# Kernel tuning notes

Hardware: AMD Instinct MI355X
Metric: run time of the kernel (lower is better)

The kernel has to match this reference:

```python
import jax, jax.numpy as jnp
import numpy as np

N, E, F, H1, H2 = 8192, 131072, 512, 32, 16
POS_WEIGHT = 10.0


def gcn_conv(x, W, src, dst, n):
    h = x @ W  # [n, out]
    deg = jax.ops.segment_sum(jnp.ones(dst.shape[0], x.dtype), dst, num_segments=n) + 1.0  # self-loop
    dinv = jnp.where(deg > 0, deg ** -0.5, 0.0)
    coef = dinv[src] * dinv[dst]  # [E]
    out = jax.ops.segment_sum(h[src] * coef[:, None], dst, num_segments=n)
    out = out + h * (dinv * dinv)[:, None]  # self-loop message
    return out


def setup_inputs() -> dict:
    key = jax.random.key(0)
    ks = jax.random.split(key, 8)
    x = jax.random.normal(ks[0], (N, F), dtype=jnp.float32)
    edge_index = jax.random.randint(ks[1], (2, E), 0, N, dtype=jnp.int32)
    adj_label = jax.random.randint(ks[2], (N, N), 0, 2, dtype=jnp.int32)
    eps = jax.random.normal(ks[3], (N, H2), dtype=jnp.float32)
    norm = jnp.ones((1,), dtype=jnp.float32)
    W1 = jax.random.normal(ks[4], (F, H1), dtype=jnp.float32) * 0.05
    W2 = jax.random.normal(ks[5], (H1, H2), dtype=jnp.float32) * 0.05
    W3 = jax.random.normal(ks[6], (H1, H2), dtype=jnp.float32) * 0.05
    return {"x": x, "edge_index": edge_index, "adj_label": adj_label,
            "eps": eps, "norm": norm, "W1": W1, "W2": W2, "W3": W3}


def reference(x, edge_index, adj_label, eps, norm, W1, W2, W3):
    n = x.shape[0]
    src, dst = edge_index[0], edge_index[1]
    h1 = jax.nn.relu(gcn_conv(x, W1, src, dst, n))
    mu = gcn_conv(h1, W2, src, dst, n)
    logvar = gcn_conv(h1, W3, src, dst, n)
    # reparameterize: std = exp(logvar) (as in source, not exp(0.5*logvar))
    z = eps * jnp.exp(logvar) + mu
    logits = z @ z.T  # [N, N] inner-product decode
    y = adj_label.astype(logits.dtype)
    # BCEWithLogitsLoss with pos_weight, numerically stable
    sp = jax.nn.softplus(-logits)
    bce = jnp.mean(POS_WEIGHT * y * sp + (1.0 - y) * (logits + sp))
    cost = norm[0] * bce
    kld = (-0.5 / n) * jnp.mean(jnp.sum(1.0 + 2.0 * logvar - mu ** 2 - jnp.exp(logvar) ** 2, axis=1))
    return cost + kld, mu
```

## Files before the change

### kernel.cpp

```cpp
#include <hip/hip_runtime.h>
#include <cstdint>
#include <cstddef>

#define N_NODES 8192
#define N_EDGES 131072
#define F_IN    512
#define H1C     32
#define H2C     16


__device__ __forceinline__ float block_reduce_sum(float v, int nthreads) {
    #pragma unroll
    for (int off = 32; off; off >>= 1) v += __shfl_down(v, off, 64);
    __shared__ float sred[16];
    int lane = threadIdx.x & 63, wid = threadIdx.x >> 6;
    if (lane == 0) sred[wid] = v;
    __syncthreads();
    float s = 0.0f;
    if (threadIdx.x == 0) {
        int nw = nthreads >> 6;
        for (int i = 0; i < nw; ++i) s += sred[i];
    }
    return s;
}

__device__ __forceinline__ float bce_elem(float l, int y) {
    float lse = __logf(1.0f + __expf(-fabsf(l)));
    float sp  = lse + fmaxf(l, 0.0f);
    float w   = (float)y;
    return fmaf(sp, fmaf(9.0f, w, 1.0f), -10.0f * w * l);
}


__global__ void k_init(float4* __restrict__ p) {
    int gid = blockIdx.x * 256 + threadIdx.x;
    float4 zz = {0.0f, 0.0f, 0.0f, 0.0f};
    p[gid] = zz;
}

__global__ void k_fill(const int* __restrict__ src, const int* __restrict__ dst,
                       int* __restrict__ cnt, int* __restrict__ csr_src) {
    int e = blockIdx.x * 256 + threadIdx.x;
    int d = dst[e], sv = src[e];
    int slot = atomicAdd(&cnt[d], 1);
    if (slot < 64) csr_src[(d << 6) + slot] = sv;
}

__global__ void __launch_bounds__(256)
k_gemm1(const float* __restrict__ x, const float* __restrict__ W1,
        float* __restrict__ h) {
    __shared__ float wsm[F_IN][H1C];
    int tid = threadIdx.x;
    {
        float4* wd = (float4*)wsm;
        const float4* wsrc = (const float4*)W1;
        #pragma unroll
        for (int i = 0; i < 16; ++i) wd[tid + i * 256] = wsrc[tid + i * 256];
    }
    __syncthreads();

    int row = (blockIdx.x << 5) + (tid >> 3);
    int c4 = (tid & 7) << 2;
    const float4* xp = (const float4*)&x[(size_t)row * F_IN];

    float ax = 0.f, ay = 0.f, az = 0.f, aw = 0.f;
    #pragma unroll 8
    for (int k4 = 0; k4 < F_IN / 4; ++k4) {
        float4 xv = xp[k4];
        float4 w0 = *(const float4*)&wsm[k4 * 4 + 0][c4];
        float4 w1 = *(const float4*)&wsm[k4 * 4 + 1][c4];
        float4 w2 = *(const float4*)&wsm[k4 * 4 + 2][c4];
        float4 w3 = *(const float4*)&wsm[k4 * 4 + 3][c4];
        ax = fmaf(xv.x, w0.x, ax); ay = fmaf(xv.x, w0.y, ay);
        az = fmaf(xv.x, w0.z, az); aw = fmaf(xv.x, w0.w, aw);
        ax = fmaf(xv.y, w1.x, ax); ay = fmaf(xv.y, w1.y, ay);
        az = fmaf(xv.y, w1.z, az); aw = fmaf(xv.y, w1.w, aw);
        ax = fmaf(xv.z, w2.x, ax); ay = fmaf(xv.z, w2.y, ay);
        az = fmaf(xv.z, w2.z, az); aw = fmaf(xv.z, w2.w, aw);
        ax = fmaf(xv.w, w3.x, ax); ay = fmaf(xv.w, w3.y, ay);
        az = fmaf(xv.w, w3.z, az); aw = fmaf(xv.w, w3.w, aw);
    }
    float4 v; v.x = ax; v.y = ay; v.z = az; v.w = aw;
    *(float4*)&h[(size_t)row * H1C + c4] = v;
}

__global__ void __launch_bounds__(256)
k_g1g2(const int* __restrict__ csr_src, const int* __restrict__ cnt,
       const float* __restrict__ h, const float* __restrict__ W2,
       const float* __restrict__ W3, float* __restrict__ h2mu,
       float* __restrict__ h2lv) {
    __shared__ float w2s[H1C * H2C], w3s[H1C * H2C];
    __shared__ float h1s[4][33];
    int tid = threadIdx.x;
    {
        w2s[tid] = W2[tid]; w2s[tid + 256] = W2[tid + 256];
        w3s[tid] = W3[tid]; w3s[tid + 256] = W3[tid + 256];
    }
    __syncthreads();

    int w = tid >> 6;
    int row = blockIdx.x * 4 + w;
    int lane = tid & 63;
    int f = lane & 31, half = lane >> 5;
    int n = min(cnt[row], 64);
    float acc = 0.0f;
    for (int sl = half; sl < n; sl += 2) {
        int s = csr_src[(row << 6) + sl];
        float c = rsqrtf((float)(cnt[s] + 1));
        acc = fmaf(h[(s << 5) + f], c, acc);
    }
    acc += __shfl_down(acc, 32, 64);
    if (half == 0) {
        float di = rsqrtf((float)(n + 1)), d2 = di * di;
        float a1 = acc * di;
        h1s[w][f] = fmaxf(fmaf(h[(row << 5) + f], d2, a1), 0.0f);
    }
    if (half == 0) {
        const float* wsrc = (f < 16) ? w2s : w3s;
        int col = f & 15;
        float o = 0.0f;
        #pragma unroll
        for (int k = 0; k < H1C; ++k) o = fmaf(h1s[w][k], wsrc[(k << 4) + col], o);
        if (f < 16) h2mu[(row << 4) + col] = o;
        else        h2lv[(row << 4) + col] = o;
    }
}

__global__ void __launch_bounds__(256)
k_g2z(const int* __restrict__ csr_src, const int* __restrict__ cnt,
      const float* __restrict__ h2mu, const float* __restrict__ h2lv,
      const float* __restrict__ eps, float* __restrict__ zbuf,
      float* __restrict__ out, float* __restrict__ kldp) {
    int tid = threadIdx.x;
    int row = blockIdx.x * 4 + (tid >> 6);
    int lane = tid & 63;
    int f = lane & 31, half = lane >> 5;
    int ff = f & 15;
    const float* hsrc = (f < 16) ? h2mu : h2lv;
    int n = min(cnt[row], 64);
    float acc = 0.0f;
    for (int sl = half; sl < n; sl += 2) {
        int s = csr_src[(row << 6) + sl];
        float c = rsqrtf((float)(cnt[s] + 1));
        acc = fmaf(hsrc[(s << 4) + ff], c, acc);
    }
    acc += __shfl_down(acc, 32, 64);
    float di = rsqrtf((float)(n + 1)), d2 = di * di;
    float val = fmaf(hsrc[(row << 4) + ff], d2, acc * di);
    float other = __shfl_xor(val, 16, 64);
    float kterm = 0.0f;
    if (half == 0 && f < 16) {
        float m = val, lv = other;
        float el = __expf(lv);
        float zv = fmaf(eps[(row << 4) + ff], el, m);
        zbuf[(row << 4) + ff] = zv;
        out[1 + (row << 4) + ff] = m;
        kterm = 1.0f + 2.0f * lv - m * m - el * el;
    }
    float bs = block_reduce_sum(kterm, 256);
    if (tid == 0) kldp[blockIdx.x] = bs;
}

__global__ void __launch_bounds__(256)
k_bce(const float* __restrict__ z, const int* __restrict__ adj,
      float* __restrict__ part) {
    __shared__ float zrT[16][32];
    int tid = threadIdx.x;
    int band = blockIdx.x & 15;
    int rblk = blockIdx.x >> 4;
    int col0 = (band << 9) + (tid << 1);
    int row0 = rblk << 5;

    if (tid < 128) {
        int r = tid >> 2, q = (tid & 3) << 2;
        float4 v = *(const float4*)&z[(size_t)(row0 + r) * H2C + q];
        zrT[q + 0][r] = v.x; zrT[q + 1][r] = v.y;
        zrT[q + 2][r] = v.z; zrT[q + 3][r] = v.w;
    }

    float zc[2][16];
    {
        const float4* zp = (const float4*)&z[(size_t)col0 * H2C];
        #pragma unroll
        for (int q = 0; q < 8; ++q) {
            float4 v = zp[q];
            int c = q >> 2, qq = (q & 3) << 2;
            zc[c][qq + 0] = v.x; zc[c][qq + 1] = v.y;
            zc[c][qq + 2] = v.z; zc[c][qq + 3] = v.w;
        }
    }
    __syncthreads();

    float lsum = 0.0f;
    #pragma unroll
    for (int step = 0; step < 8; ++step) {
        int r0 = step << 2;
        const int* ap = adj + (size_t)(row0 + r0) * N_NODES + col0;
        int2 y0 = *(const int2*)(ap);
        int2 y1 = *(const int2*)(ap + N_NODES);
        int2 y2 = *(const int2*)(ap + 2 * N_NODES);
        int2 y3 = *(const int2*)(ap + 3 * N_NODES);

        float a[4][2];
        #pragma unroll
        for (int r = 0; r < 4; ++r) { a[r][0] = 0.0f; a[r][1] = 0.0f; }
        #pragma unroll
        for (int k = 0; k < 16; ++k) {
            float4 zr4 = *(const float4*)&zrT[k][r0];
            a[0][0] = fmaf(zr4.x, zc[0][k], a[0][0]);
            a[0][1] = fmaf(zr4.x, zc[1][k], a[0][1]);
            a[1][0] = fmaf(zr4.y, zc[0][k], a[1][0]);
            a[1][1] = fmaf(zr4.y, zc[1][k], a[1][1]);
            a[2][0] = fmaf(zr4.z, zc[0][k], a[2][0]);
            a[2][1] = fmaf(zr4.z, zc[1][k], a[2][1]);
            a[3][0] = fmaf(zr4.w, zc[0][k], a[3][0]);
            a[3][1] = fmaf(zr4.w, zc[1][k], a[3][1]);
        }
        lsum += bce_elem(a[0][0], y0.x) + bce_elem(a[0][1], y0.y);
        lsum += bce_elem(a[1][0], y1.x) + bce_elem(a[1][1], y1.y);
        lsum += bce_elem(a[2][0], y2.x) + bce_elem(a[2][1], y2.y);
        lsum += bce_elem(a[3][0], y3.x) + bce_elem(a[3][1], y3.y);
    }

    float bs = block_reduce_sum(lsum, 256);
    if (tid == 0) part[blockIdx.x] = bs;
}

__global__ void k_final(const float* __restrict__ part, const float* __restrict__ kldp,
                        const float* __restrict__ norm, float* __restrict__ out) {
    double s = 0.0, k = 0.0;
    for (int i = threadIdx.x; i < 4096; i += 256) s += (double)part[i];
    for (int i = threadIdx.x; i < 2048; i += 256) k += (double)kldp[i];
    #pragma unroll
    for (int off = 32; off; off >>= 1) {
        s += __shfl_down(s, off, 64);
        k += __shfl_down(k, off, 64);
    }
    __shared__ double ss[4], kk[4];
    int lane = threadIdx.x & 63, wid = threadIdx.x >> 6;
    if (lane == 0) { ss[wid] = s; kk[wid] = k; }
    __syncthreads();
    if (threadIdx.x == 0) {
        double st = ss[0] + ss[1] + ss[2] + ss[3];
        double kt = kk[0] + kk[1] + kk[2] + kk[3];
        double bce = st / ((double)N_NODES * (double)N_NODES);
        double kld = (-0.5 / (double)N_NODES) * (kt / (double)N_NODES);
        out[0] = (float)((double)norm[0] * bce + kld);
    }
}


extern "C" void kernel_launch(void* const* d_in, const int* in_sizes, int n_in,
                              void* d_out, int out_size, void* d_ws, size_t ws_size,
                              hipStream_t stream) {
    const float* x    = (const float*)d_in[0];
    const int*   ei   = (const int*)d_in[1];
    const int*   adj  = (const int*)d_in[2];
    const float* eps  = (const float*)d_in[3];
    const float* norm = (const float*)d_in[4];
    const float* W1   = (const float*)d_in[5];
    const float* W2   = (const float*)d_in[6];
    const float* W3   = (const float*)d_in[7];
    float* out = (float*)d_out;
    char*  ws  = (char*)d_ws;

    const int* src = ei;
    const int* dst = ei + N_EDGES;

    int*   cnt     = (int*)  (ws + 0);
    int*   csr_src = (int*)  (ws + 32768);
    float* h       = (float*)(ws + 2129920);
    float* h2mu    = (float*)(ws + 3178496);
    float* h2lv    = (float*)(ws + 3702784);
    float* zbuf    = (float*)(ws + 4227072);
    float* part    = (float*)(ws + 4751360);
    float* kldp    = (float*)(ws + 4767744);

    k_init<<<8, 256, 0, stream>>>((float4*)cnt);
    k_fill<<<N_EDGES / 256, 256, 0, stream>>>(src, dst, cnt, csr_src);
    k_gemm1<<<N_NODES / 32, 256, 0, stream>>>(x, W1, h);
    k_g1g2<<<N_NODES / 4, 256, 0, stream>>>(csr_src, cnt, h, W2, W3, h2mu, h2lv);
    k_g2z<<<N_NODES / 4, 256, 0, stream>>>(csr_src, cnt, h2mu, h2lv, eps, zbuf, out, kldp);
    k_bce<<<4096, 256, 0, stream>>>(zbuf, adj, part);
    k_final<<<1, 256, 0, stream>>>(part, kldp, norm, out);
}
```

Baseline: 123.7 us.

## Fuse edge fill with first GEMM and fold final reduction into BCE kernel

Merges the CSR fill kernel into the first GEMM launch by giving extra blocks the edge-bucketing work, so the two independent stages run concurrently in one grid. Replaces the separate final reduction kernel with a last-block-done pattern in the BCE kernel, using an atomic counter and thread fences. This removes two kernel launches and their gaps, at the cost of an extra atomic per BCE block and a serial tail reduction in one block. The init kernel now also zeroes the done counter.

```diff
diff --git a/kernel.cpp b/kernel.cpp
--- a/kernel.cpp
+++ b/kernel.cpp
@@ -35,22 +35,25 @@
 __global__ void k_init(float4* __restrict__ p) {
     int gid = blockIdx.x * 256 + threadIdx.x;
     float4 zz = {0.0f, 0.0f, 0.0f, 0.0f};
-    p[gid] = zz;
-}
-
-__global__ void k_fill(const int* __restrict__ src, const int* __restrict__ dst,
-                       int* __restrict__ cnt, int* __restrict__ csr_src) {
-    int e = blockIdx.x * 256 + threadIdx.x;
-    int d = dst[e], sv = src[e];
-    int slot = atomicAdd(&cnt[d], 1);
-    if (slot < 64) csr_src[(d << 6) + slot] = sv;
-}
-
-__global__ void __launch_bounds__(256)
-k_gemm1(const float* __restrict__ x, const float* __restrict__ W1,
-        float* __restrict__ h) {
+    if (gid <= 2048) p[gid] = zz;
+}
+
+__global__ void __launch_bounds__(256)
+k_fg(const int* __restrict__ src, const int* __restrict__ dst,
+     int* __restrict__ cnt, int* __restrict__ csr_src,
+     const float* __restrict__ x, const float* __restrict__ W1,
+     float* __restrict__ h) {
     __shared__ float wsm[F_IN][H1C];
-    int tid = threadIdx.x;
+    int tid = threadIdx.x, bid = blockIdx.x;
+
+    if (bid >= 256) {
+        int e = (bid - 256) * 256 + tid;
+        int d = dst[e], sv = src[e];
+        int slot = atomicAdd(&cnt[d], 1);
+        if (slot < 64) csr_src[(d << 6) + slot] = sv;
+        return;
+    }
+
     {
         float4* wd = (float4*)wsm;
         const float4* wsrc = (const float4*)W1;
@@ -59,7 +62,7 @@
     }
     __syncthreads();
 
-    int row = (blockIdx.x << 5) + (tid >> 3);
+    int row = (bid << 5) + (tid >> 3);
     int c4 = (tid & 7) << 2;
     const float4* xp = (const float4*)&x[(size_t)row * F_IN];
 
@@ -163,7 +166,9 @@
 
 __global__ void __launch_bounds__(256)
 k_bce(const float* __restrict__ z, const int* __restrict__ adj,
-      float* __restrict__ part) {
+      float* __restrict__ part, const float* __restrict__ kldp,
+      const float* __restrict__ norm, float* __restrict__ out,
+      int* __restrict__ done) {
     __shared__ float zrT[16][32];
     int tid = threadIdx.x;
     int band = blockIdx.x & 15;
@@ -223,29 +228,34 @@
     }
 
     float bs = block_reduce_sum(lsum, 256);
-    if (tid == 0) part[blockIdx.x] = bs;
-}
-
-__global__ void k_final(const float* __restrict__ part, const float* __restrict__ kldp,
-                        const float* __restrict__ norm, float* __restrict__ out) {
-    double s = 0.0, k = 0.0;
-    for (int i = threadIdx.x; i < 4096; i += 256) s += (double)part[i];
-    for (int i = threadIdx.x; i < 2048; i += 256) k += (double)kldp[i];
-    #pragma unroll
-    for (int off = 32; off; off >>= 1) {
-        s += __shfl_down(s, off, 64);
-        k += __shfl_down(k, off, 64);
-    }
-    __shared__ double ss[4], kk[4];
-    int lane = threadIdx.x & 63, wid = threadIdx.x >> 6;
-    if (lane == 0) { ss[wid] = s; kk[wid] = k; }
-    __syncthreads();
-    if (threadIdx.x == 0) {
-        double st = ss[0] + ss[1] + ss[2] + ss[3];
-        double kt = kk[0] + kk[1] + kk[2] + kk[3];
-        double bce = st / ((double)N_NODES * (double)N_NODES);
-        double kld = (-0.5 / (double)N_NODES) * (kt / (double)N_NODES);
-        out[0] = (float)((double)norm[0] * bce + kld);
+    __shared__ int amlast;
+    if (tid == 0) {
+        part[blockIdx.x] = bs;
+        __threadfence();
+        amlast = (atomicAdd(done, 1) == 4095);
+    }
+    __syncthreads();
+    if (amlast) {
+        __threadfence();
+        double s = 0.0, k = 0.0;
+        for (int i = tid; i < 4096; i += 256) s += (double)part[i];
+        for (int i = tid; i < 2048; i += 256) k += (double)kldp[i];
+        #pragma unroll
+        for (int off = 32; off; off >>= 1) {
+            s += __shfl_down(s, off, 64);
+            k += __shfl_down(k, off, 64);
+        }
+        __shared__ double ss[4], kk[4];
+        int lane = tid & 63, wid = tid >> 6;
+        if (lane == 0) { ss[wid] = s; kk[wid] = k; }
+        __syncthreads();
+        if (tid == 0) {
+            double st = ss[0] + ss[1] + ss[2] + ss[3];
+            double kt = kk[0] + kk[1] + kk[2] + kk[3];
+            double bce = st / ((double)N_NODES * (double)N_NODES);
+            double kld = (-0.5 / (double)N_NODES) * (kt / (double)N_NODES);
+            out[0] = (float)((double)norm[0] * bce + kld);
+        }
     }
 }
 
@@ -268,19 +278,18 @@
     const int* dst = ei + N_EDGES;
 
     int*   cnt     = (int*)  (ws + 0);
-    int*   csr_src = (int*)  (ws + 32768);
-    float* h       = (float*)(ws + 2129920);
-    float* h2mu    = (float*)(ws + 3178496);
-    float* h2lv    = (float*)(ws + 3702784);
-    float* zbuf    = (float*)(ws + 4227072);
-    float* part    = (float*)(ws + 4751360);
-    float* kldp    = (float*)(ws + 4767744);
-
-    k_init<<<8, 256, 0, stream>>>((float4*)cnt);
-    k_fill<<<N_EDGES / 256, 256, 0, stream>>>(src, dst, cnt, csr_src);
-    k_gemm1<<<N_NODES / 32, 256, 0, stream>>>(x, W1, h);
+    int*   done    = (int*)  (ws + 32768);
+    int*   csr_src = (int*)  (ws + 32832);
+    float* h       = (float*)(ws + 2129984);
+    float* h2mu    = (float*)(ws + 3178560);
+    float* h2lv    = (float*)(ws + 3702848);
+    float* zbuf    = (float*)(ws + 4227136);
+    float* part    = (float*)(ws + 4751424);
+    float* kldp    = (float*)(ws + 4767808);
+
+    k_init<<<9, 256, 0, stream>>>((float4*)cnt);
+    k_fg<<<768, 256, 0, stream>>>(src, dst, cnt, csr_src, x, W1, h);
     k_g1g2<<<N_NODES / 4, 256, 0, stream>>>(csr_src, cnt, h, W2, W3, h2mu, h2lv);
     k_g2z<<<N_NODES / 4, 256, 0, stream>>>(csr_src, cnt, h2mu, h2lv, eps, zbuf, out, kldp);
-    k_bce<<<4096, 256, 0, stream>>>(zbuf, adj, part);
-    k_final<<<1, 256, 0, stream>>>(part, kldp, norm, out);
-}
+    k_bce<<<4096, 256, 0, stream>>>(zbuf, adj, part, kldp, norm, out, done);
+}
```

Result: slower. 301.9 us (+144.1%).
